# Kernel optimization log

Measured on AMD Instinct MI355X. Metric: run time of the kernel, lower is better.

Reference implementation:

```python
import jax, jax.numpy as jnp
import numpy as np

B, S, C = 2, 4096, 640
HEADS = 10
DH = C // HEADS  # 64
SCALE = 1.0 / np.sqrt(DH).astype(np.float32)


def setup_inputs() -> dict:
    key = jax.random.key(0)
    ks = jax.random.split(key, 5)
    w_std = 0.02
    return {
        "hidden_states": jax.random.normal(ks[0], (B, S, C), dtype=jnp.float32),
        "Wq": jax.random.normal(ks[1], (C, C), dtype=jnp.float32) * w_std,
        "Wk": jax.random.normal(ks[2], (C, C), dtype=jnp.float32) * w_std,
        "Wv": jax.random.normal(ks[3], (C, C), dtype=jnp.float32) * w_std,
        "Wo": jax.random.normal(ks[4], (C, C), dtype=jnp.float32) * w_std,
        "b_out": jnp.zeros((C,), dtype=jnp.float32),
    }


def _split_heads(x):
    # [B, S, C] -> [B, H, S, Dh]
    b, s, c = x.shape
    return x.reshape(b, s, HEADS, DH).transpose(0, 2, 1, 3)


def reference(hidden_states, Wq, Wk, Wv, Wo, b_out):
    residual = hidden_states
    # Linear projections (torch nn.Linear: x @ W.T), to_q/k/v have no bias
    q = jnp.einsum("bsc,dc->bsd", hidden_states, Wq)
    k = jnp.einsum("bsc,dc->bsd", hidden_states, Wk)
    v = jnp.einsum("bsc,dc->bsd", hidden_states, Wv)
    q = _split_heads(q)  # [B, H, S, Dh]
    k = _split_heads(k)
    v = _split_heads(v)
    # get_attention_scores: scaled QK^T + softmax (full O(S^2) matrix)
    scores = jnp.einsum("bhqd,bhkd->bhqk", q, k) * SCALE
    probs = jax.nn.softmax(scores, axis=-1)
    out = jnp.einsum("bhqk,bhkd->bhqd", probs, v)  # [B, H, S, Dh]
    # batch_to_head_dim: [B, H, S, Dh] -> [B, S, C]
    out = out.transpose(0, 2, 1, 3).reshape(hidden_states.shape)
    # to_out[0] Linear (with bias), to_out[1] Dropout = identity at eval
    out = jnp.einsum("bsc,dc->bsd", out, Wo) + b_out
    # residual_connection=True, rescale_output_factor=1.0
    return out + residual
```

## Files before the change

### kernel.cpp

```cpp
#include <hip/hip_runtime.h>
#include <stdint.h>
#include <stddef.h>

#define Bsz 2
#define Ssz 4096
#define Csz 640
#define Hn 10
#define Dh 64
#define NSPLIT 4
#define QROWS 81920

typedef __attribute__((ext_vector_type(8))) short bf16x8;
typedef __attribute__((ext_vector_type(4))) float f32x4;
typedef __attribute__((ext_vector_type(16))) float f32x16;

typedef __attribute__((address_space(1))) void as1_void;
typedef __attribute__((address_space(3))) void as3_void;

__device__ __forceinline__ void async16(const void* g, void* l) {
  __builtin_amdgcn_global_load_lds((as1_void*)(g), (as3_void*)(l), 16, 0, 0);
}

__device__ __forceinline__ ushort f2bf(float f) {
  union { float f; uint32_t u; } v; v.f = f;
  return (ushort)((v.u + 0x7FFFu + ((v.u >> 16) & 1u)) >> 16);
}

__device__ __forceinline__ uint32_t pack_bf16(float lo, float hi) {
  return __builtin_amdgcn_perm(__float_as_uint(hi), __float_as_uint(lo), 0x07060302u);
}

__device__ __forceinline__ float bf_lo(uint32_t u) {
  return __uint_as_float(u << 16);
}
__device__ __forceinline__ float bf_hi(uint32_t u) {
  return __uint_as_float(u & 0xFFFF0000u);
}

__device__ __forceinline__ float fast_exp2(float x) {
#if __has_builtin(__builtin_amdgcn_exp2f)
  return __builtin_amdgcn_exp2f(x);
#else
  return __exp2f(x);
#endif
}

#define QSCALE 0.1803368801111204f

__global__ __launch_bounds__(256) void cvt_bf16(const float* __restrict__ in,
                                                ushort* __restrict__ out, int n4) {
  int i = blockIdx.x * 256 + threadIdx.x;
  if (i < n4) {
    const float4 v = ((const float4*)in)[i];
    ushort4 o;
    o.x = f2bf(v.x); o.y = f2bf(v.y); o.z = f2bf(v.z); o.w = f2bf(v.w);
    ((ushort4*)out)[i] = o;
  }
}

__global__ __launch_bounds__(256) void cvt4_bf16(
    const float* __restrict__ i0, const float* __restrict__ i1,
    const float* __restrict__ i2, const float* __restrict__ i3,
    ushort* __restrict__ o0, ushort* __restrict__ o1,
    ushort* __restrict__ o2, ushort* __restrict__ o3, int n4) {
  const float* in = (blockIdx.y == 0) ? i0 : (blockIdx.y == 1) ? i1
                    : (blockIdx.y == 2) ? i2 : i3;
  ushort* out = (blockIdx.y == 0) ? o0 : (blockIdx.y == 1) ? o1
                : (blockIdx.y == 2) ? o2 : o3;
  int i = blockIdx.x * 256 + threadIdx.x;
  if (i < n4) {
    const float4 v = ((const float4*)in)[i];
    ushort4 o;
    o.x = f2bf(v.x); o.y = f2bf(v.y); o.z = f2bf(v.z); o.w = f2bf(v.w);
    ((ushort4*)out)[i] = o;
  }
}

template<int MODE>
__global__ __launch_bounds__(256) void gemm_k(
    const ushort* __restrict__ A, const ushort* __restrict__ W0,
    const ushort* __restrict__ W1, const ushort* __restrict__ W2,
    ushort* __restrict__ Qh, ushort* __restrict__ Kh, ushort* __restrict__ Vt,
    const float* __restrict__ bias, const float* __restrict__ residual,
    float* __restrict__ outf)
{
  __shared__ ushort As[128 * 64];
  __shared__ ushort Bs[128 * 64];
  const int t = threadIdx.x;
  const int lane = t & 63;
  const int w = t >> 6;
  const int quad = lane >> 4;
  const int l15 = lane & 15;
  const int m0 = blockIdx.x * 128;
  const int wub = t & ~63;

  int n0, mat;
  const ushort* W;
  if (MODE == 0) {
    mat = blockIdx.y / 5;
    n0 = (blockIdx.y % 5) * 128;
    W = (mat == 0) ? W0 : ((mat == 1) ? W1 : W2);
  } else {
    mat = 0;
    n0 = blockIdx.y * 128;
    W = W0;
  }
  const int qm = (w >> 1) * 64;
  const int qn = (w & 1) * 64;

  f32x4 acc[4][4];
  const f32x4 zero4 = {0.f, 0.f, 0.f, 0.f};
#pragma unroll
  for (int i = 0; i < 4; ++i)
#pragma unroll
    for (int j = 0; j < 4; ++j) acc[i][j] = zero4;

  for (int k0 = 0; k0 < Csz; k0 += 64) {
    __syncthreads();
#pragma unroll
    for (int s = 0; s < 4; ++s) {
      int L = s * 256 + t;
      int row = L >> 3, pc = L & 7;
      int c = pc ^ (row & 7);
      async16(A + (size_t)(m0 + row) * Csz + k0 + c * 8,
              (char*)As + (s * 256 + wub) * 16);
    }
#pragma unroll
    for (int s = 0; s < 4; ++s) {
      int L = s * 256 + t;
      int row = L >> 3, pc = L & 7;
      int c = pc ^ (row & 7);
      async16(W + (size_t)(n0 + row) * Csz + k0 + c * 8,
              (char*)Bs + (s * 256 + wub) * 16);
    }
    __syncthreads();
#pragma unroll
    for (int ks = 0; ks < 2; ++ks) {
      bf16x8 af[4], bfr[4];
#pragma unroll
      for (int i = 0; i < 4; ++i) {
        int row = qm + i * 16 + l15;
        int pc = (ks * 4 + quad) ^ (row & 7);
        af[i] = *(const bf16x8*)(As + row * 64 + pc * 8);
      }
#pragma unroll
      for (int j = 0; j < 4; ++j) {
        int row = qn + j * 16 + l15;
        int pc = (ks * 4 + quad) ^ (row & 7);
        bfr[j] = *(const bf16x8*)(Bs + row * 64 + pc * 8);
      }
#pragma unroll
      for (int i = 0; i < 4; ++i)
#pragma unroll
        for (int j = 0; j < 4; ++j)
          acc[i][j] = __builtin_amdgcn_mfma_f32_16x16x32_bf16(af[i], bfr[j], acc[i][j], 0, 0, 0);
    }
  }

  if (MODE == 0) {
    if (mat < 2) {
      ushort* __restrict__ dst = (mat == 0) ? Qh : Kh;
      const float sc = (mat == 0) ? QSCALE : 1.0f;
#pragma unroll
      for (int j = 0; j < 4; ++j) {
        int n = n0 + qn + j * 16 + l15;
        int h = n >> 6, dh = n & 63;
#pragma unroll
        for (int i = 0; i < 4; ++i) {
#pragma unroll
          for (int r = 0; r < 4; ++r) {
            int m = m0 + qm + i * 16 + quad * 4 + r;
            int b = m >> 12, sidx = m & 4095;
            dst[(((size_t)b * Hn + h) * Ssz + sidx) * Dh + dh] = f2bf(acc[i][j][r] * sc);
          }
        }
      }
    } else {
#pragma unroll
      for (int j = 0; j < 4; ++j) {
        int n = n0 + qn + j * 16 + l15;
        int h = n >> 6, dh = n & 63;
#pragma unroll
        for (int i = 0; i < 4; ++i) {
          int mb = m0 + qm + i * 16 + quad * 4;
          int b = mb >> 12, sidx = mb & 4095;
          ushort4 pk;
          pk.x = f2bf(acc[i][j][0]); pk.y = f2bf(acc[i][j][1]);
          pk.z = f2bf(acc[i][j][2]); pk.w = f2bf(acc[i][j][3]);
          *(ushort4*)(Vt + (((size_t)b * Hn + h) * Dh + dh) * Ssz + sidx) = pk;
        }
      }
    }
  } else {
#pragma unroll
    for (int j = 0; j < 4; ++j) {
      int n = n0 + qn + j * 16 + l15;
      float bs = bias[n];
#pragma unroll
      for (int i = 0; i < 4; ++i) {
#pragma unroll
        for (int r = 0; r < 4; ++r) {
          int m = m0 + qm + i * 16 + quad * 4 + r;
          size_t idx = (size_t)m * Csz + n;
          outf[idx] = acc[i][j][r] + bs + residual[idx];
        }
      }
    }
  }
}

__global__ __launch_bounds__(256, 2) void attn_k(
    const ushort* __restrict__ Qh, const ushort* __restrict__ Kh,
    const ushort* __restrict__ Vt, ushort* __restrict__ Opart,
    float* __restrict__ lpart)
{
  __shared__ ushort Ks[2][64 * 64];
  __shared__ ushort Vs[2][64 * 64];

  const int t = threadIdx.x;
  const int lane = t & 63;
  const int w = t >> 6;
  const int l31 = lane & 31;
  const int hi = lane >> 5;
  const int bh = blockIdx.y;
  const size_t qk_off = (size_t)bh * Ssz * Dh;
  const size_t v_off = (size_t)bh * Dh * Ssz;
  const int qbase = blockIdx.x * 256 + w * 64;
  const int kvbase = blockIdx.z * (Ssz / NSPLIT);

  bf16x8 qf[2][4];
#pragma unroll
  for (int qh = 0; qh < 2; ++qh) {
    int q = qbase + qh * 32 + l31;
#pragma unroll
    for (int ks = 0; ks < 4; ++ks)
      qf[qh][ks] = *(const bf16x8*)(Qh + qk_off + (size_t)q * Dh + ks * 16 + hi * 8);
  }

  f32x16 z16;
#pragma unroll
  for (int i = 0; i < 16; ++i) z16[i] = 0.f;

  f32x16 Oa[2][2];
#pragma unroll
  for (int qh = 0; qh < 2; ++qh)
#pragma unroll
    for (int mt = 0; mt < 2; ++mt) Oa[qh][mt] = z16;
  float lp[2] = {0.f, 0.f};

  const int row8 = lane >> 3;
  const int pcs = lane & 7;
#define STAGE(bi, kv)                                                          \
  {                                                                            \
    _Pragma("unroll") for (int s = 0; s < 2; ++s) {                            \
      int i = w * 2 + s;                                                       \
      int row = i * 8 + row8;                                                  \
      int c = pcs ^ (row & 7);                                                 \
      async16(Kh + qk_off + (size_t)(kvbase + (kv) + row) * Dh + c * 8,        \
              (char*)&Ks[bi][0] + i * 1024);                                   \
    }                                                                          \
    _Pragma("unroll") for (int s = 0; s < 2; ++s) {                            \
      int i = w * 2 + s;                                                       \
      int row = i * 8 + row8;                                                  \
      int c = pcs ^ (row & 7);                                                 \
      async16(Vt + v_off + (size_t)row * Ssz + kvbase + (kv) + c * 8,          \
              (char*)&Vs[bi][0] + i * 1024);                                   \
    }                                                                          \
  }

  STAGE(0, 0);

  const int NIT = (Ssz / NSPLIT) / 64;
  for (int it = 0; it < NIT; ++it) {
    const int cb = it & 1;
    asm volatile("s_barrier" ::: "memory");
    if (it + 1 < NIT) {
      STAGE(cb ^ 1, (it + 1) * 64);
      asm volatile("s_waitcnt vmcnt(4)" ::: "memory");
    } else {
      asm volatile("s_waitcnt vmcnt(0)" ::: "memory");
    }
    asm volatile("s_barrier" ::: "memory");

    const ushort* __restrict__ Kc = &Ks[cb][0];
    const ushort* __restrict__ Vc = &Vs[cb][0];

    uint32_t pk[2][2][8];
#pragma unroll
    for (int tau = 0; tau < 2; ++tau) {
      f32x16 Sq[2];
      int row = tau * 32 + l31;
#pragma unroll
      for (int ks = 0; ks < 4; ++ks) {
        int pc = (ks * 2 + hi) ^ (row & 7);
        bf16x8 kf = *(const bf16x8*)(Kc + row * 64 + pc * 8);
        Sq[0] = __builtin_amdgcn_mfma_f32_32x32x16_bf16(kf, qf[0][ks],
                                                        ks == 0 ? z16 : Sq[0], 0, 0, 0);
        Sq[1] = __builtin_amdgcn_mfma_f32_32x32x16_bf16(kf, qf[1][ks],
                                                        ks == 0 ? z16 : Sq[1], 0, 0, 0);
      }
#pragma unroll
      for (int qh = 0; qh < 2; ++qh) {
#pragma unroll
        for (int a = 0; a < 8; ++a) {
          float p0 = fast_exp2(Sq[qh][2 * a]);
          float p1 = fast_exp2(Sq[qh][2 * a + 1]);
          lp[qh] += p0 + p1;
          pk[qh][tau][a] = pack_bf16(p0, p1);
        }
      }
    }

#pragma unroll
    for (int ks2 = 0; ks2 < 4; ++ks2) {
      const int ts = ks2 >> 1;
      const int bA = (2 * ks2) & 3;
      const int bB = (2 * ks2 + 1) & 3;
      bf16x8 pf[2];
#pragma unroll
      for (int qh = 0; qh < 2; ++qh) {
        uint32_t xA0 = pk[qh][ts][2 * bA], xA1 = pk[qh][ts][2 * bA + 1];
        uint32_t xB0 = pk[qh][ts][2 * bB], xB1 = pk[qh][ts][2 * bB + 1];
        uint32_t own0 = hi ? xB0 : xA0, own1 = hi ? xB1 : xA1;
        uint32_t snd0 = hi ? xA0 : xB0, snd1 = hi ? xA1 : xB1;
        uint32_t rcv0 = (uint32_t)__shfl_xor((int)snd0, 32, 64);
        uint32_t rcv1 = (uint32_t)__shfl_xor((int)snd1, 32, 64);
        union { uint32_t u[4]; bf16x8 v; } pu;
        pu.u[0] = hi ? rcv0 : own0;
        pu.u[1] = hi ? rcv1 : own1;
        pu.u[2] = hi ? own0 : rcv0;
        pu.u[3] = hi ? own1 : rcv1;
        pf[qh] = pu.v;
      }
#pragma unroll
      for (int mt = 0; mt < 2; ++mt) {
        int row = mt * 32 + l31;
        int pc = (ks2 * 2 + hi) ^ (row & 7);
        bf16x8 vf = *(const bf16x8*)(Vc + row * 64 + pc * 8);
        Oa[0][mt] = __builtin_amdgcn_mfma_f32_32x32x16_bf16(vf, pf[0], Oa[0][mt], 0, 0, 0);
        Oa[1][mt] = __builtin_amdgcn_mfma_f32_32x32x16_bf16(vf, pf[1], Oa[1][mt], 0, 0, 0);
      }
    }
  }
#undef STAGE

  const size_t prow_base = (size_t)blockIdx.z * QROWS + (size_t)bh * Ssz;
#pragma unroll
  for (int qh = 0; qh < 2; ++qh) {
    float l_part = lp[qh];
    float l_tot = l_part + __shfl_xor(l_part, 32, 64);
    int q = qbase + qh * 32 + l31;
    if (hi == 0) lpart[prow_base + q] = l_tot;
    ushort* dst = Opart + (prow_base + q) * 64;
#pragma unroll
    for (int mt = 0; mt < 2; ++mt) {
#pragma unroll
      for (int g = 0; g < 4; ++g) {
        int dh0 = mt * 32 + 8 * g + 4 * hi;
        uint2 val;
        val.x = pack_bf16(Oa[qh][mt][4 * g + 0], Oa[qh][mt][4 * g + 1]);
        val.y = pack_bf16(Oa[qh][mt][4 * g + 2], Oa[qh][mt][4 * g + 3]);
        *(uint2*)(dst + dh0) = val;
      }
    }
  }
}

__global__ __launch_bounds__(256) void combine_k(
    const ushort* __restrict__ Opart, const float* __restrict__ lpart,
    ushort* __restrict__ attnb)
{
  int gid = blockIdx.x * 256 + threadIdx.x;
  int row = gid >> 4;
  int dh0 = (gid & 15) * 4;
  int bh = row >> 12, q = row & 4095;
  int b = bh / Hn, h = bh % Hn;
  float a0 = 0.f, a1 = 0.f, a2 = 0.f, a3 = 0.f, lsum = 0.f;
#pragma unroll
  for (int sp = 0; sp < NSPLIT; ++sp) {
    uint2 v = *(const uint2*)(Opart + ((size_t)sp * QROWS + row) * 64 + dh0);
    a0 += bf_lo(v.x); a1 += bf_hi(v.x);
    a2 += bf_lo(v.y); a3 += bf_hi(v.y);
    lsum += lpart[(size_t)sp * QROWS + row];
  }
  float inv = 1.0f / lsum;
  uint2 o;
  o.x = pack_bf16(a0 * inv, a1 * inv);
  o.y = pack_bf16(a2 * inv, a3 * inv);
  *(uint2*)(attnb + ((size_t)b * Ssz + q) * Csz + h * Dh + dh0) = o;
}

extern "C" void kernel_launch(void* const* d_in, const int* in_sizes, int n_in,
                              void* d_out, int out_size, void* d_ws, size_t ws_size,
                              hipStream_t stream) {
  (void)in_sizes; (void)n_in; (void)out_size; (void)ws_size;
  const float* hs = (const float*)d_in[0];
  const float* Wq = (const float*)d_in[1];
  const float* Wk = (const float*)d_in[2];
  const float* Wv = (const float*)d_in[3];
  const float* Wo = (const float*)d_in[4];
  const float* bo = (const float*)d_in[5];
  float* out = (float*)d_out;

  char* ws = (char*)d_ws;
  ushort* Xbf = (ushort*)(ws);
  ushort* Wqb = (ushort*)(ws + 10485760);
  ushort* Wkb = (ushort*)(ws + 10485760 + 819200);
  ushort* Wvb = (ushort*)(ws + 10485760 + 2 * 819200);
  ushort* Wob = (ushort*)(ws + 10485760 + 3 * 819200);
  ushort* Qh  = (ushort*)(ws + 13762560);
  ushort* Kh  = (ushort*)(ws + 13762560 + 10485760);
  ushort* Vt  = (ushort*)(ws + 13762560 + 2 * 10485760);
  ushort* attnb = (ushort*)(ws + 13762560 + 3 * 10485760);
  ushort* Opart = (ushort*)(ws + 55705600);
  float*  lpart = (float*)(ws + 55705600 + 41943040);

  hipLaunchKernelGGL(cvt_bf16, dim3(5120), dim3(256), 0, stream, hs, Xbf, 1310720);
  hipLaunchKernelGGL(cvt4_bf16, dim3(400, 4), dim3(256), 0, stream,
                     Wq, Wk, Wv, Wo, Wqb, Wkb, Wvb, Wob, 102400);

  hipLaunchKernelGGL((gemm_k<0>), dim3(64, 15), dim3(256), 0, stream,
                     Xbf, Wqb, Wkb, Wvb, Qh, Kh, Vt, (const float*)nullptr,
                     (const float*)nullptr, (float*)nullptr);
  hipLaunchKernelGGL(attn_k, dim3(16, 20, NSPLIT), dim3(256), 0, stream,
                     Qh, Kh, Vt, Opart, lpart);
  hipLaunchKernelGGL(combine_k, dim3(QROWS / 16), dim3(256), 0, stream,
                     Opart, lpart, attnb);
  hipLaunchKernelGGL((gemm_k<1>), dim3(64, 5), dim3(256), 0, stream,
                     attnb, Wob, (const ushort*)nullptr, (const ushort*)nullptr,
                     (ushort*)nullptr, (ushort*)nullptr, (ushort*)nullptr,
                     bo, hs, out);
}
```

Before: 249.3 us.

## Interleave PV MFMAs per S-tile, use permlane32_swap, raise occupancy to 3

The attention inner loop now runs the P·V MFMAs for each 32-key sub-tile right after its softmax exponentials, instead of buffering probabilities for both sub-tiles first. This halves the live packed-probability registers. The cross-half-wave shuffle with selects is replaced by the gfx950 permlane32_swap intrinsic, which removes the ds_bpermute traffic and the select instructions. Launch bounds now request 3 blocks per SM, trading tighter register limits and possible spills for more waves to hide latency.

```diff
diff --git a/kernel.cpp b/kernel.cpp
--- a/kernel.cpp
+++ b/kernel.cpp
@@ -13,6 +13,7 @@
 typedef __attribute__((ext_vector_type(8))) short bf16x8;
 typedef __attribute__((ext_vector_type(4))) float f32x4;
 typedef __attribute__((ext_vector_type(16))) float f32x16;
+typedef __attribute__((ext_vector_type(2))) unsigned int u32x2;
 
 typedef __attribute__((address_space(1))) void as1_void;
 typedef __attribute__((address_space(3))) void as3_void;
@@ -209,7 +210,7 @@
   }
 }
 
-__global__ __launch_bounds__(256, 2) void attn_k(
+__global__ __launch_bounds__(256, 3) void attn_k(
     const ushort* __restrict__ Qh, const ushort* __restrict__ Kh,
     const ushort* __restrict__ Vt, ushort* __restrict__ Opart,
     float* __restrict__ lpart)
@@ -285,7 +286,6 @@
     const ushort* __restrict__ Kc = &Ks[cb][0];
     const ushort* __restrict__ Vc = &Vs[cb][0];
 
-    uint32_t pk[2][2][8];
 #pragma unroll
     for (int tau = 0; tau < 2; ++tau) {
       f32x16 Sq[2];
@@ -299,6 +299,7 @@
         Sq[1] = __builtin_amdgcn_mfma_f32_32x32x16_bf16(kf, qf[1][ks],
                                                         ks == 0 ? z16 : Sq[1], 0, 0, 0);
       }
+      uint32_t pk[2][8];
 #pragma unroll
       for (int qh = 0; qh < 2; ++qh) {
 #pragma unroll
@@ -306,39 +307,35 @@
           float p0 = fast_exp2(Sq[qh][2 * a]);
           float p1 = fast_exp2(Sq[qh][2 * a + 1]);
           lp[qh] += p0 + p1;
-          pk[qh][tau][a] = pack_bf16(p0, p1);
-        }
-      }
-    }
-
-#pragma unroll
-    for (int ks2 = 0; ks2 < 4; ++ks2) {
-      const int ts = ks2 >> 1;
-      const int bA = (2 * ks2) & 3;
-      const int bB = (2 * ks2 + 1) & 3;
-      bf16x8 pf[2];
-#pragma unroll
-      for (int qh = 0; qh < 2; ++qh) {
-        uint32_t xA0 = pk[qh][ts][2 * bA], xA1 = pk[qh][ts][2 * bA + 1];
-        uint32_t xB0 = pk[qh][ts][2 * bB], xB1 = pk[qh][ts][2 * bB + 1];
-        uint32_t own0 = hi ? xB0 : xA0, own1 = hi ? xB1 : xA1;
-        uint32_t snd0 = hi ? xA0 : xB0, snd1 = hi ? xA1 : xB1;
-        uint32_t rcv0 = (uint32_t)__shfl_xor((int)snd0, 32, 64);
-        uint32_t rcv1 = (uint32_t)__shfl_xor((int)snd1, 32, 64);
-        union { uint32_t u[4]; bf16x8 v; } pu;
-        pu.u[0] = hi ? rcv0 : own0;
-        pu.u[1] = hi ? rcv1 : own1;
-        pu.u[2] = hi ? own0 : rcv0;
-        pu.u[3] = hi ? own1 : rcv1;
-        pf[qh] = pu.v;
-      }
-#pragma unroll
-      for (int mt = 0; mt < 2; ++mt) {
-        int row = mt * 32 + l31;
-        int pc = (ks2 * 2 + hi) ^ (row & 7);
-        bf16x8 vf = *(const bf16x8*)(Vc + row * 64 + pc * 8);
-        Oa[0][mt] = __builtin_amdgcn_mfma_f32_32x32x16_bf16(vf, pf[0], Oa[0][mt], 0, 0, 0);
-        Oa[1][mt] = __builtin_amdgcn_mfma_f32_32x32x16_bf16(vf, pf[1], Oa[1][mt], 0, 0, 0);
+          pk[qh][a] = pack_bf16(p0, p1);
+        }
+      }
+
+#pragma unroll
+      for (int k2 = 0; k2 < 2; ++k2) {
+        const int ks2 = tau * 2 + k2;
+        const int bA = (2 * ks2) & 3;
+        const int bB = (2 * ks2 + 1) & 3;
+        bf16x8 pf[2];
+#pragma unroll
+        for (int qh = 0; qh < 2; ++qh) {
+          u32x2 r0 = __builtin_amdgcn_permlane32_swap(pk[qh][2 * bA],
+                                                      pk[qh][2 * bB], false, false);
+          u32x2 r1 = __builtin_amdgcn_permlane32_swap(pk[qh][2 * bA + 1],
+                                                      pk[qh][2 * bB + 1], false, false);
+          union { uint32_t u[4]; bf16x8 v; } pu;
+          pu.u[0] = r0.x; pu.u[1] = r1.x;
+          pu.u[2] = r0.y; pu.u[3] = r1.y;
+          pf[qh] = pu.v;
+        }
+#pragma unroll
+        for (int mt = 0; mt < 2; ++mt) {
+          int vrow = mt * 32 + l31;
+          int pc = (ks2 * 2 + hi) ^ (vrow & 7);
+          bf16x8 vfr = *(const bf16x8*)(Vc + vrow * 64 + pc * 8);
+          Oa[0][mt] = __builtin_amdgcn_mfma_f32_32x32x16_bf16(vfr, pf[0], Oa[0][mt], 0, 0, 0);
+          Oa[1][mt] = __builtin_amdgcn_mfma_f32_32x32x16_bf16(vfr, pf[1], Oa[1][mt], 0, 0, 0);
+        }
       }
     }
   }
```

New measurement: 266.0 us. 1.07x slower.
